# Kernel tuning notes

Hardware: AMD Instinct MI355X
Metric: run time of the kernel (lower is better)

Reference implementation:

```python
import jax, jax.numpy as jnp
import numpy as np

N = 50000
E = 1_600_000
D_IN = 256
D_OUT = 256


def setup_inputs() -> dict:
    key = jax.random.key(0)
    k1, k2, k3, k4, k5 = jax.random.split(key, 5)
    x = jax.random.normal(k1, (N, D_IN), dtype=jnp.float32)
    # nn.Linear weight is [out_features, in_features], init N(0, 1/sqrt(in))
    stdv = 1.0 / np.sqrt(D_IN)
    W = jax.random.normal(k2, (D_OUT, D_IN), dtype=jnp.float32) * stdv
    edge_row = jax.random.randint(k3, (E,), 0, N, dtype=jnp.int32)
    edge_col = jax.random.randint(k4, (E,), 0, N, dtype=jnp.int32)
    # normalized adjacency values (positive, ~1/avg_degree scale)
    edge_val = jax.random.uniform(k5, (E,), dtype=jnp.float32) / 32.0
    return {"x": x, "W": W, "edge_row": edge_row, "edge_col": edge_col, "edge_val": edge_val}


def reference(x, W, edge_row, edge_col, edge_val):
    # support = input @ W.T  (nn.Linear, no bias)
    support = jnp.einsum("ni,oi->no", x, W)  # [N, D_OUT]
    # output = sparse_adj @ support : gather source rows, scale, scatter-add to dest
    msgs = support[edge_col] * edge_val[:, None]  # [E, D_OUT]
    output = jax.ops.segment_sum(msgs, edge_row, num_segments=N)  # [N, D_OUT]
    return output
```

## Files before the change

### kernel.cpp

```cpp
#include <hip/hip_runtime.h>

#define D 256
#define HIST_BLOCKS 1024
#define GEMM_ROWS 64
#define LDB 40
#define MAXDEG 96

typedef float f32x4  __attribute__((ext_vector_type(4)));
typedef short bf16x8 __attribute__((ext_vector_type(8)));

__device__ __forceinline__ unsigned short f2bf(float f) {
    unsigned u = __float_as_uint(f);
    u += 0x7fffu + ((u >> 16) & 1u);
    return (unsigned short)(u >> 16);
}
__device__ __forceinline__ float bf2f(unsigned short h) {
    return __uint_as_float(((unsigned)h) << 16);
}

__global__ __launch_bounds__(256) void hist_gemm(
        const float* __restrict__ x, const float* __restrict__ W,
        unsigned short* __restrict__ suppb, int n_rows,
        const int* __restrict__ erow, int* __restrict__ cnt,
        int* __restrict__ rank, int E) {
    __shared__ short As[GEMM_ROWS * LDB];
    __shared__ short Ws[D * LDB];

    if (blockIdx.x < HIST_BLOCKS) {
        const int stride = HIST_BLOCKS * 256;
        int e = blockIdx.x * 256 + threadIdx.x;
        for (; e + 3 * stride < E; e += 4 * stride) {
            const int d0 = erow[e];
            const int d1 = erow[e + stride];
            const int d2 = erow[e + 2 * stride];
            const int d3 = erow[e + 3 * stride];
            const int r0 = atomicAdd(&cnt[d0], 1);
            const int r1 = atomicAdd(&cnt[d1], 1);
            const int r2 = atomicAdd(&cnt[d2], 1);
            const int r3 = atomicAdd(&cnt[d3], 1);
            rank[e]              = r0;
            rank[e + stride]     = r1;
            rank[e + 2 * stride] = r2;
            rank[e + 3 * stride] = r3;
        }
        for (; e < E; e += stride)
            rank[e] = atomicAdd(&cnt[erow[e]], 1);
        return;
    }

    const int m0   = (blockIdx.x - HIST_BLOCKS) * GEMM_ROWS;
    const int t    = threadIdx.x;
    const int lane = t & 63;
    const int w    = t >> 6;
    const int fr   = lane & 15;
    const int oct  = lane >> 4;

    f32x4 acc[16];
#pragma unroll
    for (int nt = 0; nt < 16; ++nt) acc[nt] = (f32x4){0.f, 0.f, 0.f, 0.f};

    const int ar = t >> 2;
    const int ac = (t & 3) * 8;

    for (int k0 = 0; k0 < D; k0 += 32) {
        {
            const int gm = m0 + ar;
            float4 a0 = {0.f, 0.f, 0.f, 0.f}, a1 = {0.f, 0.f, 0.f, 0.f};
            if (gm < n_rows) {
                a0 = *(const float4*)(x + (size_t)gm * D + k0 + ac);
                a1 = *(const float4*)(x + (size_t)gm * D + k0 + ac + 4);
            }
            ushort4 u0, u1;
            u0.x = f2bf(a0.x); u0.y = f2bf(a0.y); u0.z = f2bf(a0.z); u0.w = f2bf(a0.w);
            u1.x = f2bf(a1.x); u1.y = f2bf(a1.y); u1.z = f2bf(a1.z); u1.w = f2bf(a1.w);
            *(ushort4*)(&As[ar * LDB + ac])     = u0;
            *(ushort4*)(&As[ar * LDB + ac + 4]) = u1;
        }
        {
            const float* src = W + (size_t)t * D + k0;
#pragma unroll
            for (int q = 0; q < 4; ++q) {
                const float4 a = *(const float4*)(src + q * 8);
                const float4 b = *(const float4*)(src + q * 8 + 4);
                ushort4 u, v;
                u.x = f2bf(a.x); u.y = f2bf(a.y); u.z = f2bf(a.z); u.w = f2bf(a.w);
                v.x = f2bf(b.x); v.y = f2bf(b.y); v.z = f2bf(b.z); v.w = f2bf(b.w);
                *(ushort4*)(&Ws[t * LDB + q * 8])     = u;
                *(ushort4*)(&Ws[t * LDB + q * 8 + 4]) = v;
            }
        }
        __syncthreads();

        const bf16x8 afrag = *(const bf16x8*)(&As[(w * 16 + fr) * LDB + oct * 8]);
#pragma unroll
        for (int nt = 0; nt < 16; ++nt) {
            const bf16x8 bfrag = *(const bf16x8*)(&Ws[(nt * 16 + fr) * LDB + oct * 8]);
            acc[nt] = __builtin_amdgcn_mfma_f32_16x16x32_bf16(afrag, bfrag, acc[nt], 0, 0, 0);
        }
        __syncthreads();
    }

#pragma unroll
    for (int nt = 0; nt < 16; ++nt) {
#pragma unroll
        for (int r = 0; r < 4; ++r) {
            const int gm = m0 + w * 16 + oct * 4 + r;
            if (gm < n_rows)
                suppb[(size_t)gm * D + nt * 16 + fr] = f2bf(acc[nt][r]);
        }
    }
}

__global__ __launch_bounds__(256) void edge_bin(
        const int* __restrict__ erow, const int* __restrict__ ecol,
        const float* __restrict__ eval, const int* __restrict__ rank,
        unsigned* __restrict__ bins, int E) {
    int e = blockIdx.x * 256 + threadIdx.x;
    const int stride = gridDim.x * 256;
    for (; e < E; e += stride) {
        const int r = rank[e];
        if (r < MAXDEG)
            bins[erow[e] * MAXDEG + r] =
                ((unsigned)f2bf(eval[e]) << 16) | (unsigned)ecol[e];
    }
}

__global__ __launch_bounds__(256) void spmm_pull(const int* __restrict__ cnt,
                                                 const unsigned int* __restrict__ bins,
                                                 const unsigned short* __restrict__ supp,
                                                 float* __restrict__ out, int n) {
    const int lane4 = (threadIdx.x & 63) * 4;
    const int row   = blockIdx.x * 4 + (threadIdx.x >> 6);
    if (row >= n) return;

    int i = row * MAXDEG;
    const int e = i + min(cnt[row], MAXDEG);
    float ax = 0.f, ay = 0.f, az = 0.f, aw = 0.f;

    for (; i + 7 < e; i += 8) {
        unsigned p[8];
        ushort4  s[8];
#pragma unroll
        for (int j = 0; j < 8; ++j) p[j] = __builtin_nontemporal_load(&bins[i + j]);
#pragma unroll
        for (int j = 0; j < 8; ++j)
            s[j] = *(const ushort4*)(supp + (size_t)(p[j] & 0xFFFFu) * D + lane4);
#pragma unroll
        for (int j = 0; j < 8; ++j) {
            const float v = bf2f((unsigned short)(p[j] >> 16));
            ax = fmaf(bf2f(s[j].x), v, ax); ay = fmaf(bf2f(s[j].y), v, ay);
            az = fmaf(bf2f(s[j].z), v, az); aw = fmaf(bf2f(s[j].w), v, aw);
        }
    }
    for (; i < e; ++i) {
        const unsigned p0 = __builtin_nontemporal_load(&bins[i]);
        const ushort4 s0 = *(const ushort4*)(supp + (size_t)(p0 & 0xFFFFu) * D + lane4);
        const float v0 = bf2f((unsigned short)(p0 >> 16));
        ax = fmaf(bf2f(s0.x), v0, ax); ay = fmaf(bf2f(s0.y), v0, ay);
        az = fmaf(bf2f(s0.z), v0, az); aw = fmaf(bf2f(s0.w), v0, aw);
    }
    float* o = out + (size_t)row * D + lane4;
    __builtin_nontemporal_store(ax, o + 0);
    __builtin_nontemporal_store(ay, o + 1);
    __builtin_nontemporal_store(az, o + 2);
    __builtin_nontemporal_store(aw, o + 3);
}

__global__ __launch_bounds__(256) void spmm_scatter(const int* __restrict__ erow,
                                                    const int* __restrict__ ecol,
                                                    const float* __restrict__ eval,
                                                    const unsigned short* __restrict__ supp,
                                                    float* __restrict__ out, int E) {
    const int lane4 = (threadIdx.x & 63) * 4;
    const int wid  = (int)((blockIdx.x * blockDim.x + threadIdx.x) >> 6);
    const int nw   = (int)((gridDim.x * blockDim.x) >> 6);
    for (int e = wid; e < E; e += nw) {
        const int   dst = erow[e];
        const int   src = ecol[e];
        const float v   = eval[e];
        const ushort4 s = *(const ushort4*)(supp + (size_t)src * D + lane4);
        float* o = out + (size_t)dst * D + lane4;
        atomicAdd(o + 0, bf2f(s.x) * v);
        atomicAdd(o + 1, bf2f(s.y) * v);
        atomicAdd(o + 2, bf2f(s.z) * v);
        atomicAdd(o + 3, bf2f(s.w) * v);
    }
}

extern "C" void kernel_launch(void* const* d_in, const int* in_sizes, int n_in,
                              void* d_out, int out_size, void* d_ws, size_t ws_size,
                              hipStream_t stream) {
    const float* x    = (const float*)d_in[0];
    const float* W    = (const float*)d_in[1];
    const int*   erow = (const int*)d_in[2];
    const int*   ecol = (const int*)d_in[3];
    const float* eval = (const float*)d_in[4];
    float*       out  = (float*)d_out;

    const int n = in_sizes[0] / D;
    const int E = in_sizes[2];
    const int nbm = (n + GEMM_ROWS - 1) / GEMM_ROWS;

    size_t off = 0;
    auto take = [&](size_t bytes) {
        char* p = (char*)d_ws + off;
        off += (bytes + 255) & ~(size_t)255;
        return (void*)p;
    };
    unsigned short* suppb = (unsigned short*)take((size_t)n * D * 2);
    int*      cnt  = (int*)take((size_t)n * sizeof(int));
    int*      rank = (int*)take((size_t)E * sizeof(int));
    unsigned* bins = (unsigned*)take((size_t)n * MAXDEG * sizeof(unsigned));
    const bool slots_ok = (off <= ws_size);

    if (slots_ok) {
        hipMemsetAsync(cnt, 0, (size_t)n * sizeof(int), stream);
        hist_gemm<<<HIST_BLOCKS + nbm, 256, 0, stream>>>(
            x, W, suppb, n, erow, cnt, rank, E);
        edge_bin<<<2048, 256, 0, stream>>>(erow, ecol, eval, rank, bins, E);
        spmm_pull<<<(n + 3) / 4, 256, 0, stream>>>(cnt, bins, suppb, out, n);
    } else {
        hipMemsetAsync(d_out, 0, (size_t)out_size * sizeof(float), stream);
        hist_gemm<<<HIST_BLOCKS + nbm, 256, 0, stream>>>(
            x, W, suppb, n, erow, (int*)d_ws, (int*)d_ws, 0);
        spmm_scatter<<<4096, 256, 0, stream>>>(erow, ecol, eval, suppb, out, E);
    }
}
```

Baseline: 250.9 us.

## Restructure kernel stages: overlap edge binning with GEMM, pre-convert W, pad counters

Splits the work into a histogram kernel that also converts W to bf16 once, followed by a kernel that runs edge binning concurrently with the GEMM blocks. The separate edge_bin launch goes away, and GEMM blocks load W already in bf16 instead of converting it per tile. Per-row counters are padded to 16 ints so atomics on different rows land on separate cache lines. The trade-off is a 16x larger counter array and memset, an extra W buffer, and the histogram no longer overlapping the GEMM.

```diff
diff --git a/kernel.cpp b/kernel.cpp
--- a/kernel.cpp
+++ b/kernel.cpp
@@ -1,10 +1,12 @@
 #include <hip/hip_runtime.h>
 
 #define D 256
-#define HIST_BLOCKS 1024
+#define HIST_BLOCKS 2048
+#define BIN_BLOCKS 1024
 #define GEMM_ROWS 64
 #define LDB 40
 #define MAXDEG 96
+#define CPAD 16
 
 typedef float f32x4  __attribute__((ext_vector_type(4)));
 typedef short bf16x8 __attribute__((ext_vector_type(8)));
@@ -18,37 +20,49 @@
     return __uint_as_float(((unsigned)h) << 16);
 }
 
-__global__ __launch_bounds__(256) void hist_gemm(
-        const float* __restrict__ x, const float* __restrict__ W,
+__global__ __launch_bounds__(256) void prep_hist_wconv(
+        const int* __restrict__ erow, int* __restrict__ cnt,
+        int* __restrict__ rank, int E,
+        const float* __restrict__ W, unsigned short* __restrict__ Wb) {
+    if (blockIdx.x < HIST_BLOCKS) {
+        int e = blockIdx.x * 256 + threadIdx.x;
+        const int stride = HIST_BLOCKS * 256;
+        for (; e < E; e += stride)
+            rank[e] = atomicAdd(&cnt[erow[e] * CPAD], 1);
+        return;
+    }
+    const int i = (blockIdx.x - HIST_BLOCKS) * 256 + threadIdx.x;
+    const float4 a = ((const float4*)W)[i * 2];
+    const float4 b = ((const float4*)W)[i * 2 + 1];
+    ushort4 lo, hi;
+    lo.x = f2bf(a.x); lo.y = f2bf(a.y); lo.z = f2bf(a.z); lo.w = f2bf(a.w);
+    hi.x = f2bf(b.x); hi.y = f2bf(b.y); hi.z = f2bf(b.z); hi.w = f2bf(b.w);
+    ((ushort4*)Wb)[i * 2]     = lo;
+    ((ushort4*)Wb)[i * 2 + 1] = hi;
+}
+
+__global__ __launch_bounds__(256) void bin_gemm(
+        const float* __restrict__ x, const unsigned short* __restrict__ Wb,
         unsigned short* __restrict__ suppb, int n_rows,
-        const int* __restrict__ erow, int* __restrict__ cnt,
-        int* __restrict__ rank, int E) {
+        const int* __restrict__ erow, const int* __restrict__ ecol,
+        const float* __restrict__ eval, const int* __restrict__ rank,
+        unsigned* __restrict__ bins, int E) {
     __shared__ short As[GEMM_ROWS * LDB];
     __shared__ short Ws[D * LDB];
 
-    if (blockIdx.x < HIST_BLOCKS) {
-        const int stride = HIST_BLOCKS * 256;
+    if (blockIdx.x < BIN_BLOCKS) {
         int e = blockIdx.x * 256 + threadIdx.x;
-        for (; e + 3 * stride < E; e += 4 * stride) {
-            const int d0 = erow[e];
-            const int d1 = erow[e + stride];
-            const int d2 = erow[e + 2 * stride];
-            const int d3 = erow[e + 3 * stride];
-            const int r0 = atomicAdd(&cnt[d0], 1);
-            const int r1 = atomicAdd(&cnt[d1], 1);
-            const int r2 = atomicAdd(&cnt[d2], 1);
-            const int r3 = atomicAdd(&cnt[d3], 1);
-            rank[e]              = r0;
-            rank[e + stride]     = r1;
-            rank[e + 2 * stride] = r2;
-            rank[e + 3 * stride] = r3;
-        }
-        for (; e < E; e += stride)
-            rank[e] = atomicAdd(&cnt[erow[e]], 1);
+        const int stride = BIN_BLOCKS * 256;
+        for (; e < E; e += stride) {
+            const int r = rank[e];
+            if (r < MAXDEG)
+                bins[erow[e] * MAXDEG + r] =
+                    ((unsigned)f2bf(eval[e]) << 16) | (unsigned)ecol[e];
+        }
         return;
     }
 
-    const int m0   = (blockIdx.x - HIST_BLOCKS) * GEMM_ROWS;
+    const int m0   = (blockIdx.x - BIN_BLOCKS) * GEMM_ROWS;
     const int t    = threadIdx.x;
     const int lane = t & 63;
     const int w    = t >> 6;
@@ -77,17 +91,15 @@
             *(ushort4*)(&As[ar * LDB + ac + 4]) = u1;
         }
         {
-            const float* src = W + (size_t)t * D + k0;
-#pragma unroll
-            for (int q = 0; q < 4; ++q) {
-                const float4 a = *(const float4*)(src + q * 8);
-                const float4 b = *(const float4*)(src + q * 8 + 4);
-                ushort4 u, v;
-                u.x = f2bf(a.x); u.y = f2bf(a.y); u.z = f2bf(a.z); u.w = f2bf(a.w);
-                v.x = f2bf(b.x); v.y = f2bf(b.y); v.z = f2bf(b.z); v.w = f2bf(b.w);
-                *(ushort4*)(&Ws[t * LDB + q * 8])     = u;
-                *(ushort4*)(&Ws[t * LDB + q * 8 + 4]) = v;
-            }
+            const unsigned short* src = Wb + (size_t)t * D + k0;
+            const uint4 q0 = ((const uint4*)src)[0];
+            const uint4 q1 = ((const uint4*)src)[1];
+            const uint4 q2 = ((const uint4*)src)[2];
+            const uint4 q3 = ((const uint4*)src)[3];
+            *(uint4*)(&Ws[t * LDB + 0])  = q0;
+            *(uint4*)(&Ws[t * LDB + 8])  = q1;
+            *(uint4*)(&Ws[t * LDB + 16]) = q2;
+            *(uint4*)(&Ws[t * LDB + 24]) = q3;
         }
         __syncthreads();
 
@@ -108,20 +120,6 @@
             if (gm < n_rows)
                 suppb[(size_t)gm * D + nt * 16 + fr] = f2bf(acc[nt][r]);
         }
-    }
-}
-
-__global__ __launch_bounds__(256) void edge_bin(
-        const int* __restrict__ erow, const int* __restrict__ ecol,
-        const float* __restrict__ eval, const int* __restrict__ rank,
-        unsigned* __restrict__ bins, int E) {
-    int e = blockIdx.x * 256 + threadIdx.x;
-    const int stride = gridDim.x * 256;
-    for (; e < E; e += stride) {
-        const int r = rank[e];
-        if (r < MAXDEG)
-            bins[erow[e] * MAXDEG + r] =
-                ((unsigned)f2bf(eval[e]) << 16) | (unsigned)ecol[e];
     }
 }
 
@@ -134,7 +132,7 @@
     if (row >= n) return;
 
     int i = row * MAXDEG;
-    const int e = i + min(cnt[row], MAXDEG);
+    const int e = i + min(cnt[row * CPAD], MAXDEG);
     float ax = 0.f, ay = 0.f, az = 0.f, aw = 0.f;
 
     for (; i + 7 < e; i += 8) {
@@ -208,21 +206,25 @@
         return (void*)p;
     };
     unsigned short* suppb = (unsigned short*)take((size_t)n * D * 2);
-    int*      cnt  = (int*)take((size_t)n * sizeof(int));
+    unsigned short* Wb    = (unsigned short*)take((size_t)D * D * 2);
+    int*      cnt  = (int*)take((size_t)n * CPAD * sizeof(int));
     int*      rank = (int*)take((size_t)E * sizeof(int));
     unsigned* bins = (unsigned*)take((size_t)n * MAXDEG * sizeof(unsigned));
     const bool slots_ok = (off <= ws_size);
 
     if (slots_ok) {
-        hipMemsetAsync(cnt, 0, (size_t)n * sizeof(int), stream);
-        hist_gemm<<<HIST_BLOCKS + nbm, 256, 0, stream>>>(
-            x, W, suppb, n, erow, cnt, rank, E);
-        edge_bin<<<2048, 256, 0, stream>>>(erow, ecol, eval, rank, bins, E);
+        hipMemsetAsync(cnt, 0, (size_t)n * CPAD * sizeof(int), stream);
+        prep_hist_wconv<<<HIST_BLOCKS + 32, 256, 0, stream>>>(
+            erow, cnt, rank, E, W, Wb);
+        bin_gemm<<<BIN_BLOCKS + nbm, 256, 0, stream>>>(
+            x, Wb, suppb, n, erow, ecol, eval, rank, bins, E);
         spmm_pull<<<(n + 3) / 4, 256, 0, stream>>>(cnt, bins, suppb, out, n);
     } else {
         hipMemsetAsync(d_out, 0, (size_t)out_size * sizeof(float), stream);
-        hist_gemm<<<HIST_BLOCKS + nbm, 256, 0, stream>>>(
-            x, W, suppb, n, erow, (int*)d_ws, (int*)d_ws, 0);
+        prep_hist_wconv<<<HIST_BLOCKS + 32, 256, 0, stream>>>(
+            erow, (int*)d_ws, (int*)d_ws, 0, W, Wb);
+        bin_gemm<<<BIN_BLOCKS + nbm, 256, 0, stream>>>(
+            x, Wb, suppb, n, erow, ecol, eval, nullptr, nullptr, 0);
         spmm_scatter<<<4096, 256, 0, stream>>>(erow, ecol, eval, suppb, out, E);
     }
 }
```

Measured after the change: 227.9 us, median of 2. 1.1x faster.
